# Performance work log

Hardware: AMD Instinct MI355X
Metric: run time of the kernel (lower is better)

## Reference

```python
import jax, jax.numpy as jnp
import numpy as np

LAMBDA_COORD = 5.0
LAMBDA_NOOBJ = 0.5


def _iou(box1, box2):
    # boxes: [..., 4] in (cx, cy, w, h) format. Matches YoloLoss.IOU:
    # returns 0 when x_right < x_left or y_bottom < y_top (strict),
    # else intersection / (area1 + area2 - intersection).
    x1, y1, w1, h1 = box1[..., 0], box1[..., 1], box1[..., 2], box1[..., 3]
    x2, y2, w2, h2 = box2[..., 0], box2[..., 1], box2[..., 2], box2[..., 3]
    x_left = jnp.maximum(x1 - w1 / 2, x2 - w2 / 2)
    y_top = jnp.maximum(y1 - h1 / 2, y2 - h2 / 2)
    x_right = jnp.minimum(x1 + w1 / 2, x2 + w2 / 2)
    y_bottom = jnp.minimum(y1 + h1 / 2, y2 + h2 / 2)
    valid = jnp.logical_and(x_right >= x_left, y_bottom >= y_top)
    inter = (x_right - x_left) * (y_bottom - y_top)
    union = w1 * h1 + w2 * h2 - inter
    safe_union = jnp.where(union == 0, 1.0, union)
    return jnp.where(valid, inter / safe_union, 0.0)


def setup_inputs() -> dict:
    key = jax.random.key(0)
    k1, k2 = jax.random.split(key)
    B, S, D = 16384, 7, 30  # D = 2*5 + 20
    y = jax.random.normal(k1, (B, S, S, D), dtype=jnp.float32)
    gt = jax.random.normal(k2, (B, S, S, D), dtype=jnp.float32)
    return {"y": y, "gt": gt}


def reference(y, gt):
    pred, target = y, gt
    batch_size = pred.shape[0]
    obj = (target[..., 4] > 0).astype(pred.dtype)      # [B,S,S]
    noobj = (target[..., 4] == 0).astype(pred.dtype)   # [B,S,S]

    # class loss (mask over class channels, indices 10:)
    class_loss = jnp.sum(obj[..., None] * (target[..., 10:] - pred[..., 10:]) ** 2)

    # no-object confidence loss (channel 4, mask before responsibility edits)
    conf_loss_no_obj = jnp.sum(noobj * (target[..., 4] - pred[..., 4]) ** 2)

    # per-cell IOU of target box vs both predicted boxes
    tbox = target[..., 0:4]
    iou1 = _iou(tbox, pred[..., 0:4])   # [B,S,S]
    iou2 = _iou(tbox, pred[..., 5:9])   # [B,S,S]

    # responsibility: keep box1 iff iou1 > iou2 (ties -> box2), as in the torch loop
    resp1 = (iou1 > iou2).astype(pred.dtype)
    m1 = obj * resp1          # box1 responsible mask
    m2 = obj * (1.0 - resp1)  # box2 responsible mask

    # object confidence loss: confidence target is the IOU of the responsible box
    conf_loss_obj = jnp.sum(m1 * (iou1 - pred[..., 4]) ** 2
                            + m2 * (iou2 - pred[..., 9]) ** 2)

    # xy loss (channels 0,1 / 5,6)
    xy_loss = jnp.sum(m1 * ((target[..., 0] - pred[..., 0]) ** 2
                            + (target[..., 1] - pred[..., 1]) ** 2)
                      + m2 * ((target[..., 0] - pred[..., 5]) ** 2
                              + (target[..., 1] - pred[..., 6]) ** 2))

    # wh loss (channels 2,3 / 7,8)
    wh_loss = jnp.sum(m1 * ((target[..., 2] - pred[..., 2]) ** 2
                            + (target[..., 3] - pred[..., 3]) ** 2)
                      + m2 * ((target[..., 2] - pred[..., 7]) ** 2
                              + (target[..., 3] - pred[..., 8]) ** 2))

    total = (LAMBDA_COORD * xy_loss + LAMBDA_COORD * wh_loss
             + conf_loss_obj + LAMBDA_NOOBJ * conf_loss_no_obj
             + class_loss) / batch_size
    return total
```

## Files before the change

kernel.cpp:

```cpp
#include <hip/hip_runtime.h>

#define LAMBDA_COORD 5.0f
#define LAMBDA_NOOBJ 0.5f
#define DD 30
#define BLOCK 128
#define CPB 128
#define TILE_FLOATS (CPB * DD)

#define EL(A, k) (((k) & 1) ? A[(k) >> 1].y : A[(k) >> 1].x)

__device__ __forceinline__ float iou_t(float tx, float ty, float tw, float th,
                                       float px, float py, float pw, float ph) {
    float xl = fmaxf(tx - tw * 0.5f, px - pw * 0.5f);
    float yt = fmaxf(ty - th * 0.5f, py - ph * 0.5f);
    float xr = fminf(tx + tw * 0.5f, px + pw * 0.5f);
    float yb = fminf(ty + th * 0.5f, py + ph * 0.5f);
    bool valid = (xr >= xl) && (yb >= yt);
    float inter = (xr - xl) * (yb - yt);
    float uni = tw * th + pw * ph - inter;
    float safe = (uni == 0.0f) ? 1.0f : uni;
    return valid ? (inter / safe) : 0.0f;
}

__global__ __launch_bounds__(BLOCK) void yolo_loss_kernel(
    const float* __restrict__ pred, const float* __restrict__ targ,
    float* __restrict__ out) {
    __shared__ __align__(16) float lds[2 * TILE_FLOATS];
    __shared__ float wpart[BLOCK / 64];

    const int tid = threadIdx.x;

    const float* bp = pred + (size_t)blockIdx.x * TILE_FLOATS;
    const float* bt = targ + (size_t)blockIdx.x * TILE_FLOATS;

    float4 v[15];
#pragma unroll
    for (int c = 0; c < 15; ++c) {
        int idx = c * BLOCK + tid;
        const float* src = (idx < 960) ? (bp + (size_t)idx * 4)
                                       : (bt + (size_t)(idx - 960) * 4);
        v[c] = *(const float4*)src;
    }
#pragma unroll
    for (int c = 0; c < 15; ++c) {
        int idx = c * BLOCK + tid;
        *(float4*)(lds + (size_t)idx * 4) = v[c];
    }
    __syncthreads();

    const float2* lp = (const float2*)lds + tid * (DD / 2);
    const float2* lt = (const float2*)(lds + TILE_FLOATS) + tid * (DD / 2);

    float2 P[15], T[15];
#pragma unroll
    for (int j = 0; j < 15; ++j) P[j] = lp[j];
#pragma unroll
    for (int j = 0; j < 15; ++j) {
        if (j == 3 || j == 4) continue;
        T[j] = lt[j];
    }

    float t4 = EL(T, 4);
    float obj = (t4 > 0.0f) ? 1.0f : 0.0f;
    float noobj = (t4 == 0.0f) ? 1.0f : 0.0f;

    float cls = 0.0f;
#pragma unroll
    for (int j = 5; j < 15; ++j) {
        float dx = T[j].x - P[j].x;
        float dy = T[j].y - P[j].y;
        cls += dx * dx + dy * dy;
    }
    cls *= obj;

    float d4 = t4 - EL(P, 4);
    float conf_noobj = noobj * d4 * d4;

    float tx = EL(T, 0), ty = EL(T, 1), tw = EL(T, 2), th = EL(T, 3);
    float p0 = EL(P, 0), p1 = EL(P, 1), p2 = EL(P, 2), p3 = EL(P, 3);
    float p4 = EL(P, 4), p5 = EL(P, 5), p6 = EL(P, 6), p7 = EL(P, 7);
    float p8 = EL(P, 8), p9 = EL(P, 9);

    float iou1 = iou_t(tx, ty, tw, th, p0, p1, p2, p3);
    float iou2 = iou_t(tx, ty, tw, th, p5, p6, p7, p8);
    float resp1 = (iou1 > iou2) ? 1.0f : 0.0f;
    float m1 = obj * resp1;
    float m2 = obj * (1.0f - resp1);

    float e1 = iou1 - p4;
    float e2 = iou2 - p9;
    float conf_obj = m1 * e1 * e1 + m2 * e2 * e2;

    float dx1 = tx - p0, dy1 = ty - p1;
    float dx2 = tx - p5, dy2 = ty - p6;
    float xy = m1 * (dx1 * dx1 + dy1 * dy1) + m2 * (dx2 * dx2 + dy2 * dy2);

    float dw1 = tw - p2, dh1 = th - p3;
    float dw2 = tw - p7, dh2 = th - p8;
    float wh = m1 * (dw1 * dw1 + dh1 * dh1) + m2 * (dw2 * dw2 + dh2 * dh2);

    float loss = LAMBDA_COORD * (xy + wh) + conf_obj + LAMBDA_NOOBJ * conf_noobj + cls;

#pragma unroll
    for (int off = 32; off > 0; off >>= 1) loss += __shfl_down(loss, off);
    if ((tid & 63) == 0) wpart[tid >> 6] = loss;
    __syncthreads();
    if (tid == 0) {
        atomicAdd(out, (wpart[0] + wpart[1]) * (1.0f / 16384.0f));
    }
}

extern "C" void kernel_launch(void* const* d_in, const int* in_sizes, int n_in,
                              void* d_out, int out_size, void* d_ws, size_t ws_size,
                              hipStream_t stream) {
    const float* pred = (const float*)d_in[0];
    const float* targ = (const float*)d_in[1];
    float* out = (float*)d_out;

    hipMemsetAsync(out, 0, sizeof(float), stream);

    const int cells = in_sizes[0] / DD;
    const int grid = cells / CPB;
    yolo_loss_kernel<<<grid, BLOCK, 0, stream>>>(pred, targ, out);
}
```

Measured before the change: 230.4 us.

## Replace LDS staging with direct box reads and coalesced float4 class sweep

Drops the full-tile LDS transpose. Each thread now reads the first 10 fields of its own cell directly from global memory to compute the IOU and box terms, and stores per-cell obj/noobj weights in LDS. The class and noobj-confidence terms are then computed in a coalesced float4 sweep over the tile, weighted per channel via a division by 30. Block size goes to 256 with an occupancy hint. The trade-off is that the strided first-pass reads are uncoalesced, and the first 10 channels are read twice, relying on cache.

```diff
diff --git a/kernel.cpp b/kernel.cpp
--- a/kernel.cpp
+++ b/kernel.cpp
@@ -3,11 +3,10 @@
 #define LAMBDA_COORD 5.0f
 #define LAMBDA_NOOBJ 0.5f
 #define DD 30
-#define BLOCK 128
-#define CPB 128
-#define TILE_FLOATS (CPB * DD)
-
-#define EL(A, k) (((k) & 1) ? A[(k) >> 1].y : A[(k) >> 1].x)
+#define BLOCK 256
+#define CPB 256
+#define TILE_F (CPB * DD)
+#define TILE_C4 (TILE_F / 4)
 
 __device__ __forceinline__ float iou_t(float tx, float ty, float tw, float th,
                                        float px, float py, float pw, float ph) {
@@ -22,91 +21,86 @@
     return valid ? (inter / safe) : 0.0f;
 }
 
-__global__ __launch_bounds__(BLOCK) void yolo_loss_kernel(
+__global__ __launch_bounds__(BLOCK, 8) void yolo_loss_kernel(
     const float* __restrict__ pred, const float* __restrict__ targ,
     float* __restrict__ out) {
-    __shared__ __align__(16) float lds[2 * TILE_FLOATS];
+    __shared__ float objL[CPB];
+    __shared__ float noobjL[CPB];
     __shared__ float wpart[BLOCK / 64];
 
     const int tid = threadIdx.x;
+    const size_t base = (size_t)blockIdx.x * TILE_F;
+    const float* bp = pred + base;
+    const float* bt = targ + base;
 
-    const float* bp = pred + (size_t)blockIdx.x * TILE_FLOATS;
-    const float* bt = targ + (size_t)blockIdx.x * TILE_FLOATS;
+    float acc = 0.0f;
 
-    float4 v[15];
-#pragma unroll
-    for (int c = 0; c < 15; ++c) {
-        int idx = c * BLOCK + tid;
-        const float* src = (idx < 960) ? (bp + (size_t)idx * 4)
-                                       : (bt + (size_t)(idx - 960) * 4);
-        v[c] = *(const float4*)src;
-    }
-#pragma unroll
-    for (int c = 0; c < 15; ++c) {
-        int idx = c * BLOCK + tid;
-        *(float4*)(lds + (size_t)idx * 4) = v[c];
+    {
+        const float2* rp = (const float2*)(bp + tid * DD);
+        const float2* rt = (const float2*)(bt + tid * DD);
+        float2 p01 = rp[0], p23 = rp[1], p45 = rp[2], p67 = rp[3], p89 = rp[4];
+        float2 t01 = rt[0], t23 = rt[1], t45 = rt[2];
+
+        float t4 = t45.x;
+        float obj = (t4 > 0.0f) ? 1.0f : 0.0f;
+        float noobj = (t4 == 0.0f) ? 1.0f : 0.0f;
+        objL[tid] = obj;
+        noobjL[tid] = LAMBDA_NOOBJ * noobj;
+
+        float tx = t01.x, ty = t01.y, tw = t23.x, th = t23.y;
+        float iou1 = iou_t(tx, ty, tw, th, p01.x, p01.y, p23.x, p23.y);
+        float iou2 = iou_t(tx, ty, tw, th, p45.y, p67.x, p67.y, p89.x);
+        float resp1 = (iou1 > iou2) ? 1.0f : 0.0f;
+        float m1 = obj * resp1;
+        float m2 = obj * (1.0f - resp1);
+
+        float e1 = iou1 - p45.x;
+        float e2 = iou2 - p89.y;
+        float conf_obj = m1 * e1 * e1 + m2 * e2 * e2;
+
+        float dx1 = tx - p01.x, dy1 = ty - p01.y;
+        float dx2 = tx - p45.y, dy2 = ty - p67.x;
+        float xy = m1 * (dx1 * dx1 + dy1 * dy1) + m2 * (dx2 * dx2 + dy2 * dy2);
+
+        float dw1 = tw - p23.x, dh1 = th - p23.y;
+        float dw2 = tw - p67.y, dh2 = th - p89.x;
+        float wh = m1 * (dw1 * dw1 + dh1 * dh1) + m2 * (dw2 * dw2 + dh2 * dh2);
+
+        acc += LAMBDA_COORD * (xy + wh) + conf_obj;
     }
     __syncthreads();
 
-    const float2* lp = (const float2*)lds + tid * (DD / 2);
-    const float2* lt = (const float2*)(lds + TILE_FLOATS) + tid * (DD / 2);
-
-    float2 P[15], T[15];
+    const float4* cp = (const float4*)bp;
+    const float4* ct = (const float4*)bt;
 #pragma unroll
-    for (int j = 0; j < 15; ++j) P[j] = lp[j];
+    for (int c = 0; c < 8; ++c) {
+        int idx = c * BLOCK + tid;
+        if (idx < TILE_C4) {
+            float4 p = cp[idx];
+            float4 t = ct[idx];
+            float pe[4] = {p.x, p.y, p.z, p.w};
+            float te[4] = {t.x, t.y, t.z, t.w};
+            int f0 = idx * 4;
 #pragma unroll
-    for (int j = 0; j < 15; ++j) {
-        if (j == 3 || j == 4) continue;
-        T[j] = lt[j];
+            for (int e = 0; e < 4; ++e) {
+                int fe = f0 + e;
+                int cell = fe / 30;
+                int ch = fe - cell * 30;
+                float d = te[e] - pe[e];
+                float w = (ch >= 10) ? objL[cell]
+                         : ((ch == 4) ? noobjL[cell] : 0.0f);
+                acc += w * d * d;
+            }
+        }
     }
 
-    float t4 = EL(T, 4);
-    float obj = (t4 > 0.0f) ? 1.0f : 0.0f;
-    float noobj = (t4 == 0.0f) ? 1.0f : 0.0f;
-
-    float cls = 0.0f;
 #pragma unroll
-    for (int j = 5; j < 15; ++j) {
-        float dx = T[j].x - P[j].x;
-        float dy = T[j].y - P[j].y;
-        cls += dx * dx + dy * dy;
-    }
-    cls *= obj;
-
-    float d4 = t4 - EL(P, 4);
-    float conf_noobj = noobj * d4 * d4;
-
-    float tx = EL(T, 0), ty = EL(T, 1), tw = EL(T, 2), th = EL(T, 3);
-    float p0 = EL(P, 0), p1 = EL(P, 1), p2 = EL(P, 2), p3 = EL(P, 3);
-    float p4 = EL(P, 4), p5 = EL(P, 5), p6 = EL(P, 6), p7 = EL(P, 7);
-    float p8 = EL(P, 8), p9 = EL(P, 9);
-
-    float iou1 = iou_t(tx, ty, tw, th, p0, p1, p2, p3);
-    float iou2 = iou_t(tx, ty, tw, th, p5, p6, p7, p8);
-    float resp1 = (iou1 > iou2) ? 1.0f : 0.0f;
-    float m1 = obj * resp1;
-    float m2 = obj * (1.0f - resp1);
-
-    float e1 = iou1 - p4;
-    float e2 = iou2 - p9;
-    float conf_obj = m1 * e1 * e1 + m2 * e2 * e2;
-
-    float dx1 = tx - p0, dy1 = ty - p1;
-    float dx2 = tx - p5, dy2 = ty - p6;
-    float xy = m1 * (dx1 * dx1 + dy1 * dy1) + m2 * (dx2 * dx2 + dy2 * dy2);
-
-    float dw1 = tw - p2, dh1 = th - p3;
-    float dw2 = tw - p7, dh2 = th - p8;
-    float wh = m1 * (dw1 * dw1 + dh1 * dh1) + m2 * (dw2 * dw2 + dh2 * dh2);
-
-    float loss = LAMBDA_COORD * (xy + wh) + conf_obj + LAMBDA_NOOBJ * conf_noobj + cls;
-
-#pragma unroll
-    for (int off = 32; off > 0; off >>= 1) loss += __shfl_down(loss, off);
-    if ((tid & 63) == 0) wpart[tid >> 6] = loss;
+    for (int off = 32; off > 0; off >>= 1) acc += __shfl_down(acc, off);
+    if ((tid & 63) == 0) wpart[tid >> 6] = acc;
     __syncthreads();
     if (tid == 0) {
-        atomicAdd(out, (wpart[0] + wpart[1]) * (1.0f / 16384.0f));
+        atomicAdd(out, (wpart[0] + wpart[1] + wpart[2] + wpart[3]) *
+                           (1.0f / 16384.0f));
     }
 }
 
```

Result: no change. 226.6 us (-1.7%).

## Load cells directly from global memory and replace atomics with two-pass reduction

Applied to the files above, without the earlier changes.

Drops the LDS staging tile and has each thread read its own cell's 30 floats straight from global memory as float2 loads. The block grows to 256 threads, and the per-block atomicAdd plus memset are replaced by a partial-sum buffer in workspace and a single-block double-precision final reduction kernel. This removes LDS traffic, a barrier and atomic contention. In exchange, the per-thread global loads are strided and poorly coalesced, and a second kernel launch is added.

```diff
diff --git a/kernel.cpp b/kernel.cpp
--- a/kernel.cpp
+++ b/kernel.cpp
@@ -3,9 +3,8 @@
 #define LAMBDA_COORD 5.0f
 #define LAMBDA_NOOBJ 0.5f
 #define DD 30
-#define BLOCK 128
-#define CPB 128
-#define TILE_FLOATS (CPB * DD)
+#define BLOCK 256
+#define NPART 3136
 
 #define EL(A, k) (((k) & 1) ? A[(k) >> 1].y : A[(k) >> 1].x)
 
@@ -22,43 +21,21 @@
     return valid ? (inter / safe) : 0.0f;
 }
 
-__global__ __launch_bounds__(BLOCK) void yolo_loss_kernel(
+__global__ __launch_bounds__(BLOCK, 4) void yolo_loss_partial(
     const float* __restrict__ pred, const float* __restrict__ targ,
-    float* __restrict__ out) {
-    __shared__ __align__(16) float lds[2 * TILE_FLOATS];
+    float* __restrict__ part) {
     __shared__ float wpart[BLOCK / 64];
 
     const int tid = threadIdx.x;
+    const size_t cell = (size_t)blockIdx.x * BLOCK + tid;
 
-    const float* bp = pred + (size_t)blockIdx.x * TILE_FLOATS;
-    const float* bt = targ + (size_t)blockIdx.x * TILE_FLOATS;
-
-    float4 v[15];
-#pragma unroll
-    for (int c = 0; c < 15; ++c) {
-        int idx = c * BLOCK + tid;
-        const float* src = (idx < 960) ? (bp + (size_t)idx * 4)
-                                       : (bt + (size_t)(idx - 960) * 4);
-        v[c] = *(const float4*)src;
-    }
-#pragma unroll
-    for (int c = 0; c < 15; ++c) {
-        int idx = c * BLOCK + tid;
-        *(float4*)(lds + (size_t)idx * 4) = v[c];
-    }
-    __syncthreads();
-
-    const float2* lp = (const float2*)lds + tid * (DD / 2);
-    const float2* lt = (const float2*)(lds + TILE_FLOATS) + tid * (DD / 2);
-
+    const float2* gp = (const float2*)(pred + cell * DD);
+    const float2* gt = (const float2*)(targ + cell * DD);
     float2 P[15], T[15];
 #pragma unroll
-    for (int j = 0; j < 15; ++j) P[j] = lp[j];
+    for (int j = 0; j < 15; ++j) P[j] = gp[j];
 #pragma unroll
-    for (int j = 0; j < 15; ++j) {
-        if (j == 3 || j == 4) continue;
-        T[j] = lt[j];
-    }
+    for (int j = 0; j < 15; ++j) T[j] = gt[j];
 
     float t4 = EL(T, 4);
     float obj = (t4 > 0.0f) ? 1.0f : 0.0f;
@@ -105,9 +82,24 @@
     for (int off = 32; off > 0; off >>= 1) loss += __shfl_down(loss, off);
     if ((tid & 63) == 0) wpart[tid >> 6] = loss;
     __syncthreads();
-    if (tid == 0) {
-        atomicAdd(out, (wpart[0] + wpart[1]) * (1.0f / 16384.0f));
-    }
+    if (tid == 0)
+        part[blockIdx.x] = wpart[0] + wpart[1] + wpart[2] + wpart[3];
+}
+
+__global__ __launch_bounds__(256, 1) void yolo_loss_final(
+    const float* __restrict__ part, float* __restrict__ out) {
+    __shared__ double dpart[4];
+    const int tid = threadIdx.x;
+
+    double s = 0.0;
+    for (int i = tid; i < NPART; i += 256) s += (double)part[i];
+#pragma unroll
+    for (int off = 32; off > 0; off >>= 1) s += __shfl_down(s, off);
+    if ((tid & 63) == 0) dpart[tid >> 6] = s;
+    __syncthreads();
+    if (tid == 0)
+        out[0] = (float)((dpart[0] + dpart[1] + dpart[2] + dpart[3]) *
+                         (1.0 / 16384.0));
 }
 
 extern "C" void kernel_launch(void* const* d_in, const int* in_sizes, int n_in,
@@ -116,10 +108,10 @@
     const float* pred = (const float*)d_in[0];
     const float* targ = (const float*)d_in[1];
     float* out = (float*)d_out;
-
-    hipMemsetAsync(out, 0, sizeof(float), stream);
+    float* part = (float*)d_ws;
 
     const int cells = in_sizes[0] / DD;
-    const int grid = cells / CPB;
-    yolo_loss_kernel<<<grid, BLOCK, 0, stream>>>(pred, targ, out);
+    const int grid = cells / BLOCK;
+    yolo_loss_partial<<<grid, BLOCK, 0, stream>>>(pred, targ, part);
+    yolo_loss_final<<<1, 256, 0, stream>>>(part, out);
 }
```

Measured after the change: 206.4 us. 10.4% less time.
